# Kernel optimization log

Measured on AMD Instinct MI355X. Metric: run time of the kernel, lower is better.

Reference implementation:

```python
import jax, jax.numpy as jnp
import numpy as np

B, S, E, H, DH = 256, 256, 384, 6, 64
NEG_INF = -1e9


def setup_inputs() -> dict:
    key = jax.random.key(0)
    ks = jax.random.split(key, 8)
    sc = 0.02
    return {
        "x": jax.random.normal(ks[0], (B, S, E), jnp.float32),
        "Wq": jax.random.normal(ks[1], (H, E, DH), jnp.float32) * sc,
        "Wk": jax.random.normal(ks[2], (H, E, DH), jnp.float32) * sc,
        "Wv": jax.random.normal(ks[3], (H, E, DH), jnp.float32) * sc,
        "Wp": jax.random.normal(ks[4], (E, E), jnp.float32) * sc,
        "bp": jnp.zeros((E,), jnp.float32),
        "W1": jax.random.normal(ks[5], (E, 4 * E), jnp.float32) * sc,
        "b1": jnp.zeros((4 * E,), jnp.float32),
        "W2": jax.random.normal(ks[6], (4 * E, E), jnp.float32) * sc,
        "b2": jnp.zeros((E,), jnp.float32),
        "g1": jnp.ones((E,), jnp.float32),
        "be1": jnp.zeros((E,), jnp.float32),
        "g2": jnp.ones((E,), jnp.float32),
        "be2": jnp.zeros((E,), jnp.float32),
    }


def _layernorm(x, g, b, eps=1e-5):
    mu = jnp.mean(x, axis=-1, keepdims=True)
    var = jnp.mean(jnp.square(x - mu), axis=-1, keepdims=True)
    return (x - mu) * jax.lax.rsqrt(var + eps) * g + b


def reference(x, Wq, Wk, Wv, Wp, bp, W1, b1, W2, b2, g1, be1, g2, be2):
    # --- pre-attention LayerNorm ---
    h = _layernorm(x, g1, be1)
    # --- multi-head causal self-attention (all heads vectorized) ---
    q = jnp.einsum('bse,hed->bhsd', h, Wq)
    k = jnp.einsum('bse,hed->bhsd', h, Wk)
    v = jnp.einsum('bse,hed->bhsd', h, Wv)
    scores = jnp.einsum('bhsd,bhtd->bhst', q, k) * (DH ** -0.5)
    causal = jnp.tril(jnp.ones((S, S), dtype=bool))
    scores = jnp.where(causal, scores, NEG_INF)
    att = jax.nn.softmax(scores, axis=-1)  # dropout = identity at eval
    o = jnp.einsum('bhst,bhtd->bhsd', att, v)
    o = o.transpose(0, 2, 1, 3).reshape(x.shape[0], S, E)  # concat heads
    x = x + (o @ Wp + bp)
    # --- FFN block ---
    h2 = _layernorm(x, g2, be2)
    ffn = jax.nn.relu(h2 @ W1 + b1) @ W2 + b2
    return x + ffn
```

## Files before the change

kernel.cpp:

```cpp
#include <hip/hip_runtime.h>
#include <hip/hip_bf16.h>
#include <stdint.h>

typedef __bf16 bf16_t;
typedef __bf16 bf16x2 __attribute__((ext_vector_type(2)));
typedef __bf16 bf16x8 __attribute__((ext_vector_type(8)));
typedef float f32x4 __attribute__((ext_vector_type(4)));

#define NB 256
#define NS 256
#define NE 384
#define NH 6
#define ND 64
#define NM (NB*NS)

__device__ __forceinline__ f32x4 mfma16(bf16x8 a, bf16x8 b, f32x4 c) {
    return __builtin_amdgcn_mfma_f32_16x16x32_bf16(a, b, c, 0, 0, 0);
}

__device__ __forceinline__ void cp16_async(const bf16_t* g, const bf16_t* l) {
    __builtin_amdgcn_global_load_lds(
        (__attribute__((address_space(1))) void*)g,
        (__attribute__((address_space(3))) void*)l, 16, 0, 0);
}

__global__ void wqkv_trans(const float* __restrict__ Wq, const float* __restrict__ Wk,
                           const float* __restrict__ Wv, bf16_t* __restrict__ Wcat)
{
    int i = blockIdx.x * 256 + threadIdx.x;
    if (i >= NH*NE*ND) return;
    int d = i & 63;
    int e = (i >> 6) % NE;
    int h = i / (NE*ND);
    int n = h*64 + d;
    Wcat[(size_t)(0*NE*NH*ND) + (size_t)n*NE + e]            = (bf16_t)Wq[i];
    Wcat[(size_t)(NE)*(NH*ND) + (size_t)(384 + n)*NE + e - (size_t)(NE)*(NH*ND)] = (bf16_t)Wk[i];
    Wcat[(size_t)(768 + n)*NE + e]                            = (bf16_t)Wv[i];
}

__global__ void wtrans(const float* __restrict__ src, bf16_t* __restrict__ dst, int K, int N)
{
    int i = blockIdx.x * 256 + threadIdx.x;
    if (i >= K*N) return;
    int k = i / N, n = i % N;
    dst[(size_t)n*K + k] = (bf16_t)src[i];
}

__global__ __launch_bounds__(256) void ln_kernel(
    const float* __restrict__ x, const float* __restrict__ g,
    const float* __restrict__ be, bf16_t* __restrict__ o)
{
    const int wave = threadIdx.x >> 6, lane = threadIdx.x & 63;
    const int row = blockIdx.x * 4 + wave;
    const float* xr = x + (size_t)row * NE;
    float v[6]; float s = 0.f, sq = 0.f;
    #pragma unroll
    for (int i = 0; i < 6; i++) { v[i] = xr[i*64 + lane]; s += v[i]; sq += v[i]*v[i]; }
    #pragma unroll
    for (int off = 32; off > 0; off >>= 1) { s += __shfl_xor(s, off); sq += __shfl_xor(sq, off); }
    const float mean = s * (1.f/NE);
    const float rstd = rsqrtf(sq * (1.f/NE) - mean*mean + 1e-5f);
    bf16_t* orow = o + (size_t)row * NE;
    #pragma unroll
    for (int i = 0; i < 6; i++) {
        int e = i*64 + lane;
        orow[e] = (bf16_t)((v[i] - mean) * rstd * g[e] + be[e]);
    }
}

template<int OUT_MODE, bool RELU>
__global__ __launch_bounds__(256, 2) void gemm_bt(
    const bf16_t* __restrict__ A, const bf16_t* __restrict__ Bt,
    void* __restrict__ outp, const float* __restrict__ bias,
    const float* __restrict__ res, int M, int N, int K)
{
    __shared__ bf16_t sA[2][128*32];
    __shared__ bf16_t sB[2][128*32];
    const int tid = threadIdx.x;
    const int wave = tid >> 6, lane = tid & 63;
    const int l15 = lane & 15, quad = lane >> 4;
    const int m0 = blockIdx.x * 128;
    const int n0 = blockIdx.y * 128;
    const int wm = wave >> 1, wn = wave & 1;

    const int srow = lane >> 2;
    const int scol = (lane & 3) * 8;
    const bf16_t* gA = A  + (size_t)(m0 + 32*wave + srow) * K + scol;
    const bf16_t* gB = Bt + (size_t)(n0 + 32*wave + srow) * K + scol;

    const f32x4 zero = {0.f, 0.f, 0.f, 0.f};
    f32x4 acc[4][4];
    #pragma unroll
    for (int a = 0; a < 4; a++)
        #pragma unroll
        for (int b = 0; b < 4; b++) acc[a][b] = zero;

    const int nk = K >> 5;
    cp16_async(gA, &sA[0][(32*wave)*32]);
    cp16_async(gA + (size_t)16*K, &sA[0][(32*wave + 16)*32]);
    cp16_async(gB, &sB[0][(32*wave)*32]);
    cp16_async(gB + (size_t)16*K, &sB[0][(32*wave + 16)*32]);

    for (int it = 0; it < nk; it++) {
        __syncthreads();
        if (it + 1 < nk) {
            int kt = (it + 1) << 5;
            int nb = (it + 1) & 1;
            cp16_async(gA + kt, &sA[nb][(32*wave)*32]);
            cp16_async(gA + (size_t)16*K + kt, &sA[nb][(32*wave + 16)*32]);
            cp16_async(gB + kt, &sB[nb][(32*wave)*32]);
            cp16_async(gB + (size_t)16*K + kt, &sB[nb][(32*wave + 16)*32]);
        }
        const int cb = it & 1;
        bf16x8 af[4], bfr[4];
        #pragma unroll
        for (int i = 0; i < 4; i++)
            af[i] = *(const bf16x8*)&sA[cb][(64*wm + 16*i + l15)*32 + quad*8];
        #pragma unroll
        for (int i = 0; i < 4; i++)
            bfr[i] = *(const bf16x8*)&sB[cb][(64*wn + 16*i + l15)*32 + quad*8];
        #pragma unroll
        for (int mi = 0; mi < 4; mi++)
            #pragma unroll
            for (int ni = 0; ni < 4; ni++)
                acc[mi][ni] = mfma16(af[mi], bfr[ni], acc[mi][ni]);
    }

    #pragma unroll
    for (int mi = 0; mi < 4; mi++) {
        #pragma unroll
        for (int ni = 0; ni < 4; ni++) {
            #pragma unroll
            for (int r = 0; r < 4; r++) {
                int gm = m0 + 64*wm + 16*mi + quad*4 + r;
                int gn = n0 + 64*wn + 16*ni + l15;
                float v = acc[mi][ni][r];
                if (bias) v += bias[gn];
                if (res)  v += res[(size_t)gm*N + gn];
                if (RELU) v = fmaxf(v, 0.f);
                if (OUT_MODE == 1) {
                    int sel = (gn >= 768) ? 2 : ((gn >= 384) ? 1 : 0);
                    int within = gn - sel*384;
                    int b = gm >> 8, s = gm & 255, h = within >> 6, d = within & 63;
                    ((bf16_t*)outp)[(size_t)sel*((size_t)NM*384) +
                                    (((size_t)b*NH + h)*NS + s)*ND + d] = (bf16_t)v;
                } else {
                    ((float*)outp)[(size_t)gm*N + gn] = v;
                }
            }
        }
    }
}

__global__ __launch_bounds__(256) void attn_kernel(
    const bf16_t* __restrict__ Qg, const bf16_t* __restrict__ Kg,
    const bf16_t* __restrict__ Vg, bf16_t* __restrict__ Og)
{
    __shared__ bf16_t sK[256*72];
    __shared__ bf16_t sVT[64*264];
    __shared__ bf16_t sQ[64*72];
    __shared__ bf16_t sS[64*264];
    __shared__ float sMax[64*4];
    __shared__ float sSum[64*4];
    __shared__ float sRowSum[64];

    const int tid = threadIdx.x;
    const int wave = tid >> 6, lane = tid & 63;
    const int l15 = lane & 15, quad = lane >> 4;
    const int bh = blockIdx.x;
    const int b = bh / NH, h = bh % NH;
    const size_t base = (size_t)bh * (NS*ND);
    const bf16_t* Qb = Qg + base;
    const bf16_t* Kb = Kg + base;
    const bf16_t* Vb = Vg + base;

    #pragma unroll
    for (int it = 0; it < 8; it++) {
        int idx = it*256 + tid;
        int t = idx >> 3, c = idx & 7;
        bf16x8 kv = *(const bf16x8*)(Kb + t*64 + c*8);
        *(bf16x8*)&sK[t*72 + c*8] = kv;
        bf16x8 vv = *(const bf16x8*)(Vb + t*64 + c*8);
        #pragma unroll
        for (int j = 0; j < 8; j++) sVT[(c*8 + j)*264 + t] = vv[j];
    }

    const int r = lane;
    const int p = wave;
    const f32x4 zero = {0.f, 0.f, 0.f, 0.f};

    for (int mt = 0; mt < 4; mt++) {
        __syncthreads();
        #pragma unroll
        for (int it = 0; it < 2; it++) {
            int idx = it*256 + tid;
            int qr = idx >> 3, c = idx & 7;
            *(bf16x8*)&sQ[qr*72 + c*8] = *(const bf16x8*)(Qb + (64*mt + qr)*64 + c*8);
        }
        __syncthreads();
        if (wave <= mt) {
            const int ct = wave;
            bf16x8 bk[2][4];
            #pragma unroll
            for (int ks = 0; ks < 2; ks++)
                #pragma unroll
                for (int ni = 0; ni < 4; ni++)
                    bk[ks][ni] = *(const bf16x8*)&sK[(64*ct + 16*ni + l15)*72 + ks*32 + quad*8];
            #pragma unroll
            for (int mi = 0; mi < 4; mi++) {
                bf16x8 a0 = *(const bf16x8*)&sQ[(16*mi + l15)*72 + quad*8];
                bf16x8 a1 = *(const bf16x8*)&sQ[(16*mi + l15)*72 + 32 + quad*8];
                f32x4 sc[4];
                #pragma unroll
                for (int ni = 0; ni < 4; ni++) sc[ni] = zero;
                #pragma unroll
                for (int ni = 0; ni < 4; ni++) sc[ni] = mfma16(a0, bk[0][ni], sc[ni]);
                #pragma unroll
                for (int ni = 0; ni < 4; ni++) sc[ni] = mfma16(a1, bk[1][ni], sc[ni]);
                #pragma unroll
                for (int ni = 0; ni < 4; ni++)
                    #pragma unroll
                    for (int rr = 0; rr < 4; rr++)
                        sS[(16*mi + quad*4 + rr)*264 + 64*ct + 16*ni + l15] =
                            (bf16_t)(sc[ni][rr] * 0.125f);
            }
        }
        __syncthreads();
        const int sg = 64*mt + r;
        float mx = -INFINITY;
        if (p <= mt) {
            #pragma unroll
            for (int c = 0; c < 8; c++) {
                bf16x8 v8 = *(const bf16x8*)&sS[r*264 + 64*p + c*8];
                #pragma unroll
                for (int j = 0; j < 8; j++) {
                    int t = 64*p + c*8 + j;
                    float v = (float)v8[j];
                    mx = (t <= sg) ? fmaxf(mx, v) : mx;
                }
            }
        }
        sMax[r*4 + p] = mx;
        __syncthreads();
        const float rmax = fmaxf(fmaxf(sMax[r*4+0], sMax[r*4+1]),
                                 fmaxf(sMax[r*4+2], sMax[r*4+3]));
        float sum = 0.f;
        if (p <= mt) {
            #pragma unroll
            for (int c = 0; c < 8; c++) {
                bf16x8 v8 = *(const bf16x8*)&sS[r*264 + 64*p + c*8];
                bf16x8 e8;
                #pragma unroll
                for (int j = 0; j < 8; j++) {
                    int t = 64*p + c*8 + j;
                    float e = 0.f;
                    if (t <= sg) e = __expf((float)v8[j] - rmax);
                    sum += e;
                    e8[j] = (bf16_t)e;
                }
                *(bf16x8*)&sS[r*264 + 64*p + c*8] = e8;
            }
        }
        sSum[r*4 + p] = sum;
        __syncthreads();
        if (p == 0) sRowSum[r] = sSum[r*4+0] + sSum[r*4+1] + sSum[r*4+2] + sSum[r*4+3];
        __syncthreads();
        f32x4 oacc[4];
        #pragma unroll
        for (int ni = 0; ni < 4; ni++) oacc[ni] = zero;
        for (int kt = 0; kt <= mt; kt++) {
            bf16x8 a = *(const bf16x8*)&sS[(16*p + l15)*264 + 64*kt + quad*8];
            #pragma unroll
            for (int ni = 0; ni < 4; ni++) {
                bf16x8 bv = *(const bf16x8*)&sVT[(16*ni + l15)*264 + 64*kt + quad*8];
                oacc[ni] = mfma16(a, bv, oacc[ni]);
            }
        }
        #pragma unroll
        for (int ni = 0; ni < 4; ni++) {
            #pragma unroll
            for (int rr = 0; rr < 4; rr++) {
                int lrow = 16*p + quad*4 + rr;
                float inv = 1.0f / sRowSum[lrow];
                int srow_g = 64*mt + lrow;
                int d = 16*ni + l15;
                Og[((size_t)(b*NS + srow_g))*NE + h*ND + d] = (bf16_t)(oacc[ni][rr] * inv);
            }
        }
    }
}

__global__ __launch_bounds__(256, 1) void ffn_fused(
    float* __restrict__ xio,
    const float* __restrict__ g, const float* __restrict__ be,
    const bf16_t* __restrict__ W1t,
    const bf16_t* __restrict__ W2t,
    const float* __restrict__ b1, const float* __restrict__ b2)
{
    __shared__ bf16_t sH2[12*64*32];
    __shared__ bf16_t sW[24576];
    __shared__ bf16_t sP[2*64*32];

    const int tid = threadIdx.x;
    const int wave = tid >> 6, lane = tid & 63;
    const int l15 = lane & 15, quad = lane >> 4;
    const int wm = wave >> 1, wn = wave & 1;
    const int m0 = blockIdx.x * 64;

    for (int i = 0; i < 16; i++) {
        const int rl = wave*16 + i;
        const float* xr = xio + (size_t)(m0 + rl) * NE;
        float2 v[3]; float s = 0.f, sq = 0.f;
        #pragma unroll
        for (int j = 0; j < 3; j++) {
            v[j] = *(const float2*)(xr + j*128 + lane*2);
            s += v[j].x + v[j].y; sq += v[j].x*v[j].x + v[j].y*v[j].y;
        }
        #pragma unroll
        for (int off = 32; off > 0; off >>= 1) { s += __shfl_xor(s, off); sq += __shfl_xor(sq, off); }
        const float mean = s * (1.f/NE);
        const float rstd = rsqrtf(sq * (1.f/NE) - mean*mean + 1e-5f);
        #pragma unroll
        for (int j = 0; j < 3; j++) {
            int col = j*128 + lane*2;
            float2 gg = *(const float2*)(g + col);
            float2 bb = *(const float2*)(be + col);
            bf16x2 h2;
            h2[0] = (bf16_t)((v[j].x - mean) * rstd * gg.x + bb.x);
            h2[1] = (bf16_t)((v[j].y - mean) * rstd * gg.y + bb.y);
            *(bf16x2*)&sH2[((col >> 5)*64 + rl)*32 + (col & 31)] = h2;
        }
    }

    const f32x4 zero = {0.f, 0.f, 0.f, 0.f};
    f32x4 acc2[2][12];
    #pragma unroll
    for (int mi = 0; mi < 2; mi++)
        #pragma unroll
        for (int ni = 0; ni < 12; ni++) acc2[mi][ni] = zero;

    for (int fc = 0; fc < 24; fc++) {
        const int f0 = fc * 64;
        __syncthreads();
        for (int sg = wave; sg < 48; sg += 4) {
            int kc = sg >> 2, n = (sg & 3)*16 + (lane >> 2);
            cp16_async(W1t + (size_t)(f0 + n)*384 + kc*32 + (lane & 3)*8, &sW[sg*512]);
        }
        __syncthreads();
        f32x4 acc1[2][2];
        acc1[0][0] = zero; acc1[0][1] = zero; acc1[1][0] = zero; acc1[1][1] = zero;
        #pragma unroll
        for (int kc = 0; kc < 12; kc++) {
            bf16x8 a0 = *(const bf16x8*)&sH2[(kc*64 + 32*wm + l15)*32 + quad*8];
            bf16x8 a1 = *(const bf16x8*)&sH2[(kc*64 + 32*wm + 16 + l15)*32 + quad*8];
            bf16x8 b0 = *(const bf16x8*)&sW[(kc*64 + 32*wn + l15)*32 + quad*8];
            bf16x8 b1v = *(const bf16x8*)&sW[(kc*64 + 32*wn + 16 + l15)*32 + quad*8];
            acc1[0][0] = mfma16(a0, b0,  acc1[0][0]);
            acc1[0][1] = mfma16(a0, b1v, acc1[0][1]);
            acc1[1][0] = mfma16(a1, b0,  acc1[1][0]);
            acc1[1][1] = mfma16(a1, b1v, acc1[1][1]);
        }
        #pragma unroll
        for (int mi = 0; mi < 2; mi++)
            #pragma unroll
            for (int ni = 0; ni < 2; ni++)
                #pragma unroll
                for (int rr = 0; rr < 4; rr++) {
                    int m = 32*wm + 16*mi + quad*4 + rr;
                    int fl = 32*wn + 16*ni + l15;
                    float v = acc1[mi][ni][rr] + b1[f0 + fl];
                    v = fmaxf(v, 0.f);
                    sP[(wn*64 + m)*32 + 16*ni + l15] = (bf16_t)v;
                }
        __syncthreads();
        for (int sg = wave; sg < 48; sg += 4) {
            int kc2 = (sg >= 24) ? 1 : 0;
            int e = (sg - kc2*24)*16 + (lane >> 2);
            cp16_async(W2t + (size_t)e*1536 + f0 + kc2*32 + (lane & 3)*8, &sW[sg*512]);
        }
        __syncthreads();
        bf16x8 pa[2][2];
        #pragma unroll
        for (int kc2 = 0; kc2 < 2; kc2++)
            #pragma unroll
            for (int mi = 0; mi < 2; mi++)
                pa[kc2][mi] = *(const bf16x8*)&sP[(kc2*64 + 32*wm + 16*mi + l15)*32 + quad*8];
        #pragma unroll
        for (int ni = 0; ni < 12; ni++) {
            bf16x8 w20 = *(const bf16x8*)&sW[(0*384 + 192*wn + 16*ni + l15)*32 + quad*8];
            bf16x8 w21 = *(const bf16x8*)&sW[(1*384 + 192*wn + 16*ni + l15)*32 + quad*8];
            acc2[0][ni] = mfma16(pa[0][0], w20, acc2[0][ni]);
            acc2[0][ni] = mfma16(pa[1][0], w21, acc2[0][ni]);
            acc2[1][ni] = mfma16(pa[0][1], w20, acc2[1][ni]);
            acc2[1][ni] = mfma16(pa[1][1], w21, acc2[1][ni]);
        }
    }

    #pragma unroll
    for (int mi = 0; mi < 2; mi++) {
        #pragma unroll
        for (int ni = 0; ni < 12; ni++) {
            #pragma unroll
            for (int rr = 0; rr < 4; rr++) {
                int m = 32*wm + 16*mi + quad*4 + rr;
                int col = 192*wn + 16*ni + l15;
                size_t gi = (size_t)(m0 + m)*NE + col;
                xio[gi] = acc2[mi][ni][rr] + b2[col] + xio[gi];
            }
        }
    }
}

extern "C" void kernel_launch(void* const* d_in, const int* in_sizes, int n_in,
                              void* d_out, int out_size, void* d_ws, size_t ws_size,
                              hipStream_t stream)
{
    (void)in_sizes; (void)n_in; (void)out_size; (void)ws_size;
    const float* x   = (const float*)d_in[0];
    const float* Wq  = (const float*)d_in[1];
    const float* Wk  = (const float*)d_in[2];
    const float* Wv  = (const float*)d_in[3];
    const float* Wp  = (const float*)d_in[4];
    const float* bp  = (const float*)d_in[5];
    const float* W1  = (const float*)d_in[6];
    const float* b1  = (const float*)d_in[7];
    const float* W2  = (const float*)d_in[8];
    const float* b2  = (const float*)d_in[9];
    const float* g1  = (const float*)d_in[10];
    const float* be1 = (const float*)d_in[11];
    const float* g2  = (const float*)d_in[12];
    const float* be2 = (const float*)d_in[13];
    float* out = (float*)d_out;

    char* ws = (char*)d_ws;
    const size_t SZ = (size_t)NM * NE * 2;
    bf16_t* h_bf  = (bf16_t*)(ws);
    bf16_t* q_bf  = (bf16_t*)(ws + SZ);
    bf16_t* k_bf  = (bf16_t*)(ws + 2*SZ);
    bf16_t* v_bf  = (bf16_t*)(ws + 3*SZ);
    bf16_t* o_bf  = (bf16_t*)(ws);
    char* wb = ws + 4*SZ;
    bf16_t* Wcat = (bf16_t*)(wb);
    bf16_t* Wpt  = (bf16_t*)(wb + 884736);
    bf16_t* W1t  = (bf16_t*)(wb + 884736 + 294912);
    bf16_t* W2t  = (bf16_t*)(wb + 884736 + 294912 + 1179648);

    wqkv_trans<<<(NH*NE*ND + 255)/256, 256, 0, stream>>>(Wq, Wk, Wv, Wcat);
    wtrans<<<(NE*NE + 255)/256, 256, 0, stream>>>(Wp, Wpt, NE, NE);
    wtrans<<<(NE*4*NE + 255)/256, 256, 0, stream>>>(W1, W1t, NE, 4*NE);
    wtrans<<<(NE*4*NE + 255)/256, 256, 0, stream>>>(W2, W2t, 4*NE, NE);

    ln_kernel<<<NM/4, 256, 0, stream>>>(x, g1, be1, h_bf);

    dim3 gqkv(NM/128, 9), g384(NM/128, 3);
    gemm_bt<1,false><<<gqkv, 256, 0, stream>>>(h_bf, Wcat, q_bf, nullptr, nullptr, NM, 1152, NE);

    attn_kernel<<<NB*NH, 256, 0, stream>>>(q_bf, k_bf, v_bf, o_bf);

    gemm_bt<2,false><<<g384, 256, 0, stream>>>(o_bf, Wpt, out, bp, x, NM, NE, NE);

    ffn_fused<<<NM/64, 256, 0, stream>>>(out, g2, be2, W1t, W2t, b1, b2);
}
```

Before: 1.029 ms.

## Replace fused FFN kernel with LayerNorm plus split tiled GEMMs through bf16 hidden buffer

Removes the monolithic ffn_fused kernel, which ran one block per 64 rows with heavy LDS use and reloaded weights for every row block. The FFN now runs as a separate LayerNorm pass followed by two halves of W1-GEMM (bias+ReLU, bf16 output) and W2-GEMM (residual accumulate into out), using the existing 128x128 tiled GEMM with a new leading-dimension parameter. This gains better occupancy and tile reuse in exchange for writing and reading a 768-wide bf16 hidden activation through global memory and for extra launches.

After: 1.005 ms. 1.02x faster.

```diff
diff --git a/kernel.cpp b/kernel.cpp
--- a/kernel.cpp
+++ b/kernel.cpp
@@ -72,7 +72,7 @@
 __global__ __launch_bounds__(256, 2) void gemm_bt(
     const bf16_t* __restrict__ A, const bf16_t* __restrict__ Bt,
     void* __restrict__ outp, const float* __restrict__ bias,
-    const float* __restrict__ res, int M, int N, int K)
+    const float* __restrict__ res, int M, int N, int K, int ldb)
 {
     __shared__ bf16_t sA[2][128*32];
     __shared__ bf16_t sB[2][128*32];
@@ -86,7 +86,7 @@
     const int srow = lane >> 2;
     const int scol = (lane & 3) * 8;
     const bf16_t* gA = A  + (size_t)(m0 + 32*wave + srow) * K + scol;
-    const bf16_t* gB = Bt + (size_t)(n0 + 32*wave + srow) * K + scol;
+    const bf16_t* gB = Bt + (size_t)(n0 + 32*wave + srow) * ldb + scol;
 
     const f32x4 zero = {0.f, 0.f, 0.f, 0.f};
     f32x4 acc[4][4];
@@ -99,7 +99,7 @@
     cp16_async(gA, &sA[0][(32*wave)*32]);
     cp16_async(gA + (size_t)16*K, &sA[0][(32*wave + 16)*32]);
     cp16_async(gB, &sB[0][(32*wave)*32]);
-    cp16_async(gB + (size_t)16*K, &sB[0][(32*wave + 16)*32]);
+    cp16_async(gB + (size_t)16*ldb, &sB[0][(32*wave + 16)*32]);
 
     for (int it = 0; it < nk; it++) {
         __syncthreads();
@@ -109,7 +109,7 @@
             cp16_async(gA + kt, &sA[nb][(32*wave)*32]);
             cp16_async(gA + (size_t)16*K + kt, &sA[nb][(32*wave + 16)*32]);
             cp16_async(gB + kt, &sB[nb][(32*wave)*32]);
-            cp16_async(gB + (size_t)16*K + kt, &sB[nb][(32*wave + 16)*32]);
+            cp16_async(gB + (size_t)16*ldb + kt, &sB[nb][(32*wave + 16)*32]);
         }
         const int cb = it & 1;
         bf16x8 af[4], bfr[4];
@@ -144,8 +144,10 @@
                     int b = gm >> 8, s = gm & 255, h = within >> 6, d = within & 63;
                     ((bf16_t*)outp)[(size_t)sel*((size_t)NM*384) +
                                     (((size_t)b*NH + h)*NS + s)*ND + d] = (bf16_t)v;
+                } else if (OUT_MODE == 2) {
+                    ((float*)outp)[(size_t)gm*N + gn] = v;
                 } else {
-                    ((float*)outp)[(size_t)gm*N + gn] = v;
+                    ((bf16_t*)outp)[(size_t)gm*N + gn] = (bf16_t)v;
                 }
             }
         }
@@ -285,127 +287,6 @@
                 int srow_g = 64*mt + lrow;
                 int d = 16*ni + l15;
                 Og[((size_t)(b*NS + srow_g))*NE + h*ND + d] = (bf16_t)(oacc[ni][rr] * inv);
-            }
-        }
-    }
-}
-
-__global__ __launch_bounds__(256, 1) void ffn_fused(
-    float* __restrict__ xio,
-    const float* __restrict__ g, const float* __restrict__ be,
-    const bf16_t* __restrict__ W1t,
-    const bf16_t* __restrict__ W2t,
-    const float* __restrict__ b1, const float* __restrict__ b2)
-{
-    __shared__ bf16_t sH2[12*64*32];
-    __shared__ bf16_t sW[24576];
-    __shared__ bf16_t sP[2*64*32];
-
-    const int tid = threadIdx.x;
-    const int wave = tid >> 6, lane = tid & 63;
-    const int l15 = lane & 15, quad = lane >> 4;
-    const int wm = wave >> 1, wn = wave & 1;
-    const int m0 = blockIdx.x * 64;
-
-    for (int i = 0; i < 16; i++) {
-        const int rl = wave*16 + i;
-        const float* xr = xio + (size_t)(m0 + rl) * NE;
-        float2 v[3]; float s = 0.f, sq = 0.f;
-        #pragma unroll
-        for (int j = 0; j < 3; j++) {
-            v[j] = *(const float2*)(xr + j*128 + lane*2);
-            s += v[j].x + v[j].y; sq += v[j].x*v[j].x + v[j].y*v[j].y;
-        }
-        #pragma unroll
-        for (int off = 32; off > 0; off >>= 1) { s += __shfl_xor(s, off); sq += __shfl_xor(sq, off); }
-        const float mean = s * (1.f/NE);
-        const float rstd = rsqrtf(sq * (1.f/NE) - mean*mean + 1e-5f);
-        #pragma unroll
-        for (int j = 0; j < 3; j++) {
-            int col = j*128 + lane*2;
-            float2 gg = *(const float2*)(g + col);
-            float2 bb = *(const float2*)(be + col);
-            bf16x2 h2;
-            h2[0] = (bf16_t)((v[j].x - mean) * rstd * gg.x + bb.x);
-            h2[1] = (bf16_t)((v[j].y - mean) * rstd * gg.y + bb.y);
-            *(bf16x2*)&sH2[((col >> 5)*64 + rl)*32 + (col & 31)] = h2;
-        }
-    }
-
-    const f32x4 zero = {0.f, 0.f, 0.f, 0.f};
-    f32x4 acc2[2][12];
-    #pragma unroll
-    for (int mi = 0; mi < 2; mi++)
-        #pragma unroll
-        for (int ni = 0; ni < 12; ni++) acc2[mi][ni] = zero;
-
-    for (int fc = 0; fc < 24; fc++) {
-        const int f0 = fc * 64;
-        __syncthreads();
-        for (int sg = wave; sg < 48; sg += 4) {
-            int kc = sg >> 2, n = (sg & 3)*16 + (lane >> 2);
-            cp16_async(W1t + (size_t)(f0 + n)*384 + kc*32 + (lane & 3)*8, &sW[sg*512]);
-        }
-        __syncthreads();
-        f32x4 acc1[2][2];
-        acc1[0][0] = zero; acc1[0][1] = zero; acc1[1][0] = zero; acc1[1][1] = zero;
-        #pragma unroll
-        for (int kc = 0; kc < 12; kc++) {
-            bf16x8 a0 = *(const bf16x8*)&sH2[(kc*64 + 32*wm + l15)*32 + quad*8];
-            bf16x8 a1 = *(const bf16x8*)&sH2[(kc*64 + 32*wm + 16 + l15)*32 + quad*8];
-            bf16x8 b0 = *(const bf16x8*)&sW[(kc*64 + 32*wn + l15)*32 + quad*8];
-            bf16x8 b1v = *(const bf16x8*)&sW[(kc*64 + 32*wn + 16 + l15)*32 + quad*8];
-            acc1[0][0] = mfma16(a0, b0,  acc1[0][0]);
-            acc1[0][1] = mfma16(a0, b1v, acc1[0][1]);
-            acc1[1][0] = mfma16(a1, b0,  acc1[1][0]);
-            acc1[1][1] = mfma16(a1, b1v, acc1[1][1]);
-        }
-        #pragma unroll
-        for (int mi = 0; mi < 2; mi++)
-            #pragma unroll
-            for (int ni = 0; ni < 2; ni++)
-                #pragma unroll
-                for (int rr = 0; rr < 4; rr++) {
-                    int m = 32*wm + 16*mi + quad*4 + rr;
-                    int fl = 32*wn + 16*ni + l15;
-                    float v = acc1[mi][ni][rr] + b1[f0 + fl];
-                    v = fmaxf(v, 0.f);
-                    sP[(wn*64 + m)*32 + 16*ni + l15] = (bf16_t)v;
-                }
-        __syncthreads();
-        for (int sg = wave; sg < 48; sg += 4) {
-            int kc2 = (sg >= 24) ? 1 : 0;
-            int e = (sg - kc2*24)*16 + (lane >> 2);
-            cp16_async(W2t + (size_t)e*1536 + f0 + kc2*32 + (lane & 3)*8, &sW[sg*512]);
-        }
-        __syncthreads();
-        bf16x8 pa[2][2];
-        #pragma unroll
-        for (int kc2 = 0; kc2 < 2; kc2++)
-            #pragma unroll
-            for (int mi = 0; mi < 2; mi++)
-                pa[kc2][mi] = *(const bf16x8*)&sP[(kc2*64 + 32*wm + 16*mi + l15)*32 + quad*8];
-        #pragma unroll
-        for (int ni = 0; ni < 12; ni++) {
-            bf16x8 w20 = *(const bf16x8*)&sW[(0*384 + 192*wn + 16*ni + l15)*32 + quad*8];
-            bf16x8 w21 = *(const bf16x8*)&sW[(1*384 + 192*wn + 16*ni + l15)*32 + quad*8];
-            acc2[0][ni] = mfma16(pa[0][0], w20, acc2[0][ni]);
-            acc2[0][ni] = mfma16(pa[1][0], w21, acc2[0][ni]);
-            acc2[1][ni] = mfma16(pa[0][1], w20, acc2[1][ni]);
-            acc2[1][ni] = mfma16(pa[1][1], w21, acc2[1][ni]);
-        }
-    }
-
-    #pragma unroll
-    for (int mi = 0; mi < 2; mi++) {
-        #pragma unroll
-        for (int ni = 0; ni < 12; ni++) {
-            #pragma unroll
-            for (int rr = 0; rr < 4; rr++) {
-                int m = 32*wm + 16*mi + quad*4 + rr;
-                int col = 192*wn + 16*ni + l15;
-                size_t gi = (size_t)(m0 + m)*NE + col;
-                xio[gi] = acc2[mi][ni][rr] + b2[col] + xio[gi];
             }
         }
     }
@@ -439,6 +320,8 @@
     bf16_t* k_bf  = (bf16_t*)(ws + 2*SZ);
     bf16_t* v_bf  = (bf16_t*)(ws + 3*SZ);
     bf16_t* o_bf  = (bf16_t*)(ws);
+    bf16_t* h2_bf = (bf16_t*)(ws);
+    bf16_t* hid   = (bf16_t*)(ws + SZ);
     char* wb = ws + 4*SZ;
     bf16_t* Wcat = (bf16_t*)(wb);
     bf16_t* Wpt  = (bf16_t*)(wb + 884736);
@@ -452,12 +335,18 @@
 
     ln_kernel<<<NM/4, 256, 0, stream>>>(x, g1, be1, h_bf);
 
-    dim3 gqkv(NM/128, 9), g384(NM/128, 3);
-    gemm_bt<1,false><<<gqkv, 256, 0, stream>>>(h_bf, Wcat, q_bf, nullptr, nullptr, NM, 1152, NE);
+    dim3 gqkv(NM/128, 9), g384(NM/128, 3), gffn(NM/128, 6);
+    gemm_bt<1,false><<<gqkv, 256, 0, stream>>>(h_bf, Wcat, q_bf, nullptr, nullptr, NM, 1152, NE, NE);
 
     attn_kernel<<<NB*NH, 256, 0, stream>>>(q_bf, k_bf, v_bf, o_bf);
 
-    gemm_bt<2,false><<<g384, 256, 0, stream>>>(o_bf, Wpt, out, bp, x, NM, NE, NE);
-
-    ffn_fused<<<NM/64, 256, 0, stream>>>(out, g2, be2, W1t, W2t, b1, b2);
-}
+    gemm_bt<2,false><<<g384, 256, 0, stream>>>(o_bf, Wpt, out, bp, x, NM, NE, NE, NE);
+
+    ln_kernel<<<NM/4, 256, 0, stream>>>(out, g2, be2, h2_bf);
+
+    gemm_bt<3,true ><<<gffn, 256, 0, stream>>>(h2_bf, W1t, hid, b1, nullptr, NM, 768, NE, NE);
+    gemm_bt<2,false><<<g384, 256, 0, stream>>>(hid, W2t, out, b2, out, NM, NE, 768, 1536);
+
+    gemm_bt<3,true ><<<gffn, 256, 0, stream>>>(h2_bf, W1t + (size_t)768*NE, hid, b1 + 768, nullptr, NM, 768, NE, NE);
+    gemm_bt<2,false><<<g384, 256, 0, stream>>>(hid, W2t + 768, out, nullptr, out, NM, NE, 768, 1536);
+}
```
